# Optimization experiments

Measured on AMD Instinct MI355X. Metric: run time of the kernel, lower is better.

## Reference

```python
import jax, jax.numpy as jnp
import numpy as np

EMBED = 256
HEADS = 8
HEAD_DIM = EMBED // HEADS
LEVELS = 4
POINTS = 4
QUERY_DIM = 128
NQ = QUERY_DIM * QUERY_DIM
HIDDEN = 512
CHANNELS = [24, 40, 112, 1280]
SHAPES = [(64, 64), (32, 32), (16, 16), (8, 8)]
EPS = 1e-5


def group_norm(x, g, b, groups=32, eps=EPS):
    B, C, H, W = x.shape
    xr = x.reshape(B, groups, C // groups, H, W)
    mu = xr.mean(axis=(2, 3, 4), keepdims=True)
    var = xr.var(axis=(2, 3, 4), keepdims=True)
    xn = ((xr - mu) / jnp.sqrt(var + eps)).reshape(B, C, H, W)
    return xn * g[:, None, None] + b[:, None, None]


def layer_norm(x, g, b, eps=EPS):
    mu = x.mean(-1, keepdims=True)
    var = x.var(-1, keepdims=True)
    return (x - mu) / jnp.sqrt(var + eps) * g + b


def _sample_level(v, loc):
    # v: (B, H8, hd, H, W) value for one level; loc: (B, nq, H8, P, 2) in [0,1]
    B, Hh, hd, H, W = v.shape
    nq, P = loc.shape[1], loc.shape[3]
    # grid_sample semantics, align_corners=False, zero padding
    x = loc[..., 0] * W - 0.5
    y = loc[..., 1] * H - 0.5
    x0 = jnp.floor(x)
    y0 = jnp.floor(y)
    dx = x - x0
    dy = y - y0
    x0i = x0.astype(jnp.int32)
    y0i = y0.astype(jnp.int32)
    vflat = v.reshape(B, Hh, hd, H * W)

    def gather(xi, yi):
        valid = ((xi >= 0) & (xi < W) & (yi >= 0) & (yi < H)).astype(v.dtype)
        idx = jnp.clip(yi, 0, H - 1) * W + jnp.clip(xi, 0, W - 1)
        idxr = idx.transpose(0, 2, 1, 3).reshape(B, Hh, 1, nq * P)
        g = jnp.take_along_axis(vflat, idxr, axis=3).reshape(B, Hh, hd, nq, P)
        return g * valid.transpose(0, 2, 1, 3)[:, :, None]

    g00 = gather(x0i, y0i)
    g01 = gather(x0i + 1, y0i)
    g10 = gather(x0i, y0i + 1)
    g11 = gather(x0i + 1, y0i + 1)
    wx = dx.transpose(0, 2, 1, 3)[:, :, None]  # (B,H8,1,nq,P)
    wy = dy.transpose(0, 2, 1, 3)[:, :, None]
    return g00 * (1 - wx) * (1 - wy) + g01 * wx * (1 - wy) + g10 * (1 - wx) * wy + g11 * wx * wy


def reference(Q, grd0, grd1, grd2, grd3, batch_size,
              proj_w0, proj_b0, gn_g0, gn_b0,
              proj_w1, proj_b1, gn_g1, gn_b1,
              proj_w2, proj_b2, gn_g2, gn_b2,
              proj_w3, proj_b3, gn_g3, gn_b3,
              value_w, value_b, off_w, off_b, attw_w, attw_b,
              out_w, out_b, lin1_w, lin1_b, lin2_w, lin2_b, ln_g, ln_b):
    grd = [grd0, grd1, grd2, grd3]
    proj_w = [proj_w0, proj_w1, proj_w2, proj_w3]
    proj_b = [proj_b0, proj_b1, proj_b2, proj_b3]
    gn_g = [gn_g0, gn_g1, gn_g2, gn_g3]
    gn_b = [gn_b0, gn_b1, gn_b2, gn_b3]

    B = Q.shape[0]
    # project each level to embed dims (1x1 conv + GroupNorm) and flatten
    feats = []
    for l in range(LEVELS):
        f = jnp.einsum('bchw,co->bohw', grd[l], proj_w[l]) + proj_b[l][:, None, None]
        f = group_norm(f, gn_g[l], gn_b[l])
        feats.append(f.reshape(B, EMBED, -1).transpose(0, 2, 1))  # (B, H*W, E)
    value = jnp.concatenate(feats, axis=1)  # (B, NV, E)

    # reference points: meshgrid 'xy' over linspace(0,1,query_dim), shape (1,nq,1,2)
    lin = jnp.linspace(0.0, 1.0, QUERY_DIM)
    gx, gy = jnp.meshgrid(lin, lin, indexing='xy')
    ref = jnp.stack([gx, gy], axis=-1).reshape(1, NQ, 1, 2)

    # MSDeformAttn (mmcv): value proj, sampling offsets, attention weights
    v = (value @ value_w + value_b).reshape(B, -1, HEADS, HEAD_DIM)
    offs = (Q @ off_w + off_b).reshape(B, NQ, HEADS, LEVELS, POINTS, 2)
    aw = (Q @ attw_w + attw_b).reshape(B, NQ, HEADS, LEVELS * POINTS)
    aw = jax.nn.softmax(aw, axis=-1).reshape(B, NQ, HEADS, LEVELS, POINTS)

    # offset normalizer: (W, H) per level
    norm = jnp.array([[w, h] for (h, w) in SHAPES], dtype=Q.dtype)  # (L,2)
    # sampling_locations: (B,nq,H8,L,P,2); ref broadcasts over heads/levels/points
    loc = ref[:, :, None, :, None, :] + offs / norm[None, None, None, :, None, :]

    starts = np.concatenate([[0], np.cumsum([h * w for h, w in SHAPES])])
    out = jnp.zeros((B, HEADS, HEAD_DIM, NQ), dtype=Q.dtype)
    for l, (H, W) in enumerate(SHAPES):
        vl = v[:, starts[l]:starts[l + 1]].transpose(0, 2, 3, 1).reshape(B, HEADS, HEAD_DIM, H, W)
        sampled = _sample_level(vl, loc[:, :, :, l])  # (B,H8,hd,nq,P)
        out = out + jnp.einsum('bhdqp,bqhp->bhdq', sampled, aw[:, :, :, l])
    attn = out.transpose(0, 3, 1, 2).reshape(B, NQ, EMBED)
    attn = attn @ out_w + out_b
    attn = attn + Q  # mmcv internal residual (dropout is identity in eval)

    fused = attn + Q
    ffn = layer_norm(jax.nn.relu(fused @ lin1_w + lin1_b) @ lin2_w + lin2_b, ln_g, ln_b)
    return fused + ffn


def setup_inputs() -> dict:
    key = jax.random.key(0)
    ks = jax.random.split(key, 40)
    B = 4
    d = {
        'Q': jax.random.normal(ks[0], (B, NQ, EMBED), jnp.float32),
        'grd0': jax.random.normal(ks[1], (B, 24, 64, 64), jnp.float32),
        'grd1': jax.random.normal(ks[2], (B, 40, 32, 32), jnp.float32),
        'grd2': jax.random.normal(ks[3], (B, 112, 16, 16), jnp.float32),
        'grd3': jax.random.normal(ks[4], (B, 1280, 8, 8), jnp.float32),
        'batch_size': B,
    }
    i = 5
    for l, c in enumerate(CHANNELS):
        d[f'proj_w{l}'] = jax.random.normal(ks[i], (c, EMBED), jnp.float32) * (1.0 / np.sqrt(c)); i += 1
        d[f'proj_b{l}'] = jnp.zeros((EMBED,), jnp.float32)
        d[f'gn_g{l}'] = jnp.ones((EMBED,), jnp.float32)
        d[f'gn_b{l}'] = jnp.zeros((EMBED,), jnp.float32)

    def lin(k, fin, fout, scale=1.0):
        return jax.random.normal(k, (fin, fout), jnp.float32) * (scale / np.sqrt(fin))

    d['value_w'] = lin(ks[i], EMBED, EMBED); i += 1
    d['value_b'] = jnp.zeros((EMBED,), jnp.float32)
    d['off_w'] = lin(ks[i], EMBED, HEADS * LEVELS * POINTS * 2, 0.1); i += 1
    d['off_b'] = jnp.zeros((HEADS * LEVELS * POINTS * 2,), jnp.float32)
    d['attw_w'] = lin(ks[i], EMBED, HEADS * LEVELS * POINTS); i += 1
    d['attw_b'] = jnp.zeros((HEADS * LEVELS * POINTS,), jnp.float32)
    d['out_w'] = lin(ks[i], EMBED, EMBED); i += 1
    d['out_b'] = jnp.zeros((EMBED,), jnp.float32)
    d['lin1_w'] = lin(ks[i], EMBED, HIDDEN); i += 1
    d['lin1_b'] = jnp.zeros((HIDDEN,), jnp.float32)
    d['lin2_w'] = lin(ks[i], HIDDEN, EMBED); i += 1
    d['lin2_b'] = jnp.zeros((EMBED,), jnp.float32)
    d['ln_g'] = jnp.ones((EMBED,), jnp.float32)
    d['ln_b'] = jnp.zeros((EMBED,), jnp.float32)
    return d
```

## Files before the change

kernel.cpp:

```cpp
#include <hip/hip_runtime.h>
#include <hip/hip_bf16.h>


#define NQc 16384
#define NVc 5440

typedef __attribute__((ext_vector_type(8))) short short8;
typedef __attribute__((ext_vector_type(4))) short short4v;
typedef __attribute__((ext_vector_type(4))) float f32x4;

__device__ __forceinline__ float wred(float v) {
#pragma unroll
  for (int o = 32; o > 0; o >>= 1) v += __shfl_down(v, o);
  return v;
}

__global__ __launch_bounds__(256) void tcast_kernel(
    const float* __restrict__ w, __hip_bfloat16* __restrict__ wt, int K, int N) {
  int i = blockIdx.x * 256 + threadIdx.x;
  if (i < K * N) {
    int k = i / N, n = i - k * N;
    wt[(size_t)n * K + k] = __float2bfloat16(w[i]);
  }
}

__global__ __launch_bounds__(256) void proj_kernel(
    const float* __restrict__ g0, const float* __restrict__ g1,
    const float* __restrict__ g2, const float* __restrict__ g3,
    const float* __restrict__ w0, const float* __restrict__ w1,
    const float* __restrict__ w2, const float* __restrict__ w3,
    const float* __restrict__ pb0, const float* __restrict__ pb1,
    const float* __restrict__ pb2, const float* __restrict__ pb3,
    float* __restrict__ val) {
  const int bid = blockIdx.x;
  const int b = bid / NVc;
  const int nv = bid - b * NVc;
  const float* gsrc; const float* w; const float* pb; int C, HW, hw;
  if (nv < 4096)      { gsrc = g0; w = w0; pb = pb0; C = 24;   HW = 4096; hw = nv; }
  else if (nv < 5120) { gsrc = g1; w = w1; pb = pb1; C = 40;   HW = 1024; hw = nv - 4096; }
  else if (nv < 5376) { gsrc = g2; w = w2; pb = pb2; C = 112;  HW = 256;  hw = nv - 5120; }
  else                { gsrc = g3; w = w3; pb = pb3; C = 1280; HW = 64;   hw = nv - 5376; }
  const int e = threadIdx.x;
  const float* gp = gsrc + (size_t)b * C * HW + hw;
  float a0 = 0.f, a1 = 0.f, a2 = 0.f, a3 = 0.f;
  for (int c = 0; c < C; c += 4) {
    float x0 = gp[(size_t)(c + 0) * HW];
    float x1 = gp[(size_t)(c + 1) * HW];
    float x2 = gp[(size_t)(c + 2) * HW];
    float x3 = gp[(size_t)(c + 3) * HW];
    a0 += x0 * w[(c + 0) * 256 + e];
    a1 += x1 * w[(c + 1) * 256 + e];
    a2 += x2 * w[(c + 2) * 256 + e];
    a3 += x3 * w[(c + 3) * 256 + e];
  }
  val[(size_t)bid * 256 + e] = (a0 + a1) + (a2 + a3) + pb[e];
}

__global__ __launch_bounds__(256) void gn_kernel(
    const float* __restrict__ val, __hip_bfloat16* __restrict__ valb,
    const float* __restrict__ gg0, const float* __restrict__ gb0,
    const float* __restrict__ gg1, const float* __restrict__ gb1,
    const float* __restrict__ gg2, const float* __restrict__ gb2,
    const float* __restrict__ gg3, const float* __restrict__ gb3) {
  const int bid = blockIdx.x;
  const int grp = bid & 31;
  const int l = (bid >> 5) & 3;
  const int b = bid >> 7;
  int HW, start; const float *gg, *gbeta;
  if (l == 0)      { HW = 4096; start = 0;    gg = gg0; gbeta = gb0; }
  else if (l == 1) { HW = 1024; start = 4096; gg = gg1; gbeta = gb1; }
  else if (l == 2) { HW = 256;  start = 5120; gg = gg2; gbeta = gb2; }
  else             { HW = 64;   start = 5376; gg = gg3; gbeta = gb3; }
  const int n = HW * 8;
  const size_t base = ((size_t)(b * NVc + start)) * 256 + grp * 8;
  float s = 0.f, s2 = 0.f;
  for (int i = threadIdx.x; i < n; i += 256) {
    float x = val[base + (size_t)(i >> 3) * 256 + (i & 7)];
    s += x; s2 += x * x;
  }
  s = wred(s); s2 = wred(s2);
  __shared__ float red[8];
  const int wv = threadIdx.x >> 6;
  if ((threadIdx.x & 63) == 0) { red[wv] = s; red[4 + wv] = s2; }
  __syncthreads();
  const float S = red[0] + red[1] + red[2] + red[3];
  const float S2 = red[4] + red[5] + red[6] + red[7];
  const float inv_n = 1.f / (float)n;
  const float mu = S * inv_n;
  const float var = S2 * inv_n - mu * mu;
  const float rstd = rsqrtf(var + 1e-5f);
  for (int i = threadIdx.x; i < n; i += 256) {
    const int j = i & 7;
    const int e = grp * 8 + j;
    const size_t idx = base + (size_t)(i >> 3) * 256 + j;
    const float y = (val[idx] - mu) * rstd * gg[e] + gbeta[e];
    valb[idx] = __float2bfloat16(y);
  }
}

template <int MODE, bool XF32>
__global__ __launch_bounds__(256) void gemm_bt(
    const void* __restrict__ Xv, const __hip_bfloat16* __restrict__ Wt,
    const float* __restrict__ bias, float* __restrict__ Cf,
    __hip_bfloat16* __restrict__ Cb, const float* __restrict__ Qres,
    int M, int N, int K) {
  const int m0 = blockIdx.x * 128;
  const int n0 = blockIdx.y * 128;
  const int tid = threadIdx.x;
  const int wave = tid >> 6;
  const int lane = tid & 63;
  const int wm = wave >> 1;
  const int wn = wave & 1;
  const int l15 = lane & 15;
  const int l4 = lane >> 4;
  __shared__ __align__(16) __hip_bfloat16 As[128 * 64];
  __shared__ __align__(16) __hip_bfloat16 Bs[128 * 64];
  f32x4 acc[4][4];
#pragma unroll
  for (int m = 0; m < 4; ++m)
#pragma unroll
    for (int n = 0; n < 4; ++n) acc[m][n] = (f32x4){0.f, 0.f, 0.f, 0.f};

  for (int k0 = 0; k0 < K; k0 += 64) {
#pragma unroll
    for (int j = 0; j < 4; ++j) {
      const int e = (j * 256 + tid) * 8;
      const int r = e >> 6;
      const int k = e & 63;
      if constexpr (XF32) {
        const float* Xf = (const float*)Xv;
        const float4 a = *reinterpret_cast<const float4*>(&Xf[(size_t)(m0 + r) * K + k0 + k]);
        const float4 b = *reinterpret_cast<const float4*>(&Xf[(size_t)(m0 + r) * K + k0 + k + 4]);
        union { __hip_bfloat16 h[8]; short8 v; } u;
        u.h[0] = __float2bfloat16(a.x); u.h[1] = __float2bfloat16(a.y);
        u.h[2] = __float2bfloat16(a.z); u.h[3] = __float2bfloat16(a.w);
        u.h[4] = __float2bfloat16(b.x); u.h[5] = __float2bfloat16(b.y);
        u.h[6] = __float2bfloat16(b.z); u.h[7] = __float2bfloat16(b.w);
        *reinterpret_cast<short8*>(&As[e]) = u.v;
      } else {
        const __hip_bfloat16* Xb = (const __hip_bfloat16*)Xv;
        *reinterpret_cast<short8*>(&As[e]) =
            *reinterpret_cast<const short8*>(&Xb[(size_t)(m0 + r) * K + k0 + k]);
      }
      *reinterpret_cast<short8*>(&Bs[e]) =
          *reinterpret_cast<const short8*>(&Wt[(size_t)(n0 + r) * K + k0 + k]);
    }
    __syncthreads();
#pragma unroll
    for (int ks = 0; ks < 2; ++ks) {
      short8 a[4], bfr[4];
#pragma unroll
      for (int m = 0; m < 4; ++m)
        a[m] = *reinterpret_cast<const short8*>(
            &As[(wm * 64 + m * 16 + l15) * 64 + ks * 32 + l4 * 8]);
#pragma unroll
      for (int n = 0; n < 4; ++n)
        bfr[n] = *reinterpret_cast<const short8*>(
            &Bs[(wn * 64 + n * 16 + l15) * 64 + ks * 32 + l4 * 8]);
#pragma unroll
      for (int m = 0; m < 4; ++m)
#pragma unroll
        for (int n = 0; n < 4; ++n)
          acc[m][n] = __builtin_amdgcn_mfma_f32_16x16x32_bf16(a[m], bfr[n], acc[m][n], 0, 0, 0);
    }
    __syncthreads();
  }

#pragma unroll
  for (int m = 0; m < 4; ++m) {
    const int row0 = m0 + wm * 64 + m * 16 + l4 * 4;
#pragma unroll
    for (int n = 0; n < 4; ++n) {
      const int col = n0 + wn * 64 + n * 16 + l15;
      const float bv = bias[col];
#pragma unroll
      for (int r = 0; r < 4; ++r) {
        const size_t ci = (size_t)(row0 + r) * N + col;
        float f = acc[m][n][r] + bv;
        if (MODE == 0) {
          Cf[ci] = f;
        } else if (MODE == 1) {
          Cb[ci] = __float2bfloat16(fmaxf(f, 0.f));
        } else if (MODE == 2) {
          f += 2.f * Qres[ci];
          Cf[ci] = f;
          Cb[ci] = __float2bfloat16(f);
        } else {
          Cb[ci] = __float2bfloat16(f);
        }
      }
    }
  }
}

__global__ __launch_bounds__(256) void softmax_kernel(float* __restrict__ aw) {
  const size_t t = (size_t)blockIdx.x * 256 + threadIdx.x;
  float* p = aw + t * 16;
  float v[16];
  *reinterpret_cast<float4*>(&v[0])  = *reinterpret_cast<const float4*>(p + 0);
  *reinterpret_cast<float4*>(&v[4])  = *reinterpret_cast<const float4*>(p + 4);
  *reinterpret_cast<float4*>(&v[8])  = *reinterpret_cast<const float4*>(p + 8);
  *reinterpret_cast<float4*>(&v[12]) = *reinterpret_cast<const float4*>(p + 12);
  float mx = v[0];
#pragma unroll
  for (int j = 1; j < 16; ++j) mx = fmaxf(mx, v[j]);
  float sum = 0.f;
#pragma unroll
  for (int j = 0; j < 16; ++j) { v[j] = __expf(v[j] - mx); sum += v[j]; }
  const float inv = 1.f / sum;
#pragma unroll
  for (int j = 0; j < 16; ++j) v[j] *= inv;
  *reinterpret_cast<float4*>(p + 0)  = *reinterpret_cast<const float4*>(&v[0]);
  *reinterpret_cast<float4*>(p + 4)  = *reinterpret_cast<const float4*>(&v[4]);
  *reinterpret_cast<float4*>(p + 8)  = *reinterpret_cast<const float4*>(&v[8]);
  *reinterpret_cast<float4*>(p + 12) = *reinterpret_cast<const float4*>(&v[12]);
}

__global__ __launch_bounds__(256) void sampler_kernel(
    const float* __restrict__ V, const float* __restrict__ OFFS,
    const float* __restrict__ AW, __hip_bfloat16* __restrict__ ATT) {
  __shared__ int   sIdx[512 * 4];
  __shared__ float sW[512 * 4];
  const int blk = blockIdx.x;
  const int b = blk >> 12;
  const int q0 = (blk & 4095) << 2;
  const int bid0 = blk << 2;

  for (int j = threadIdx.x; j < 512; j += 256) {
    const int q   = j >> 7;
    const int h   = (j >> 4) & 7;
    const int tap = j & 15;
    const int l = tap >> 2, p = tap & 3;
    const int gq = bid0 + q;
    const int qq = q0 + q;
    const float rx = (float)(qq & 127) * (1.f / 127.f);
    const float ry = (float)(qq >> 7) * (1.f / 127.f);
    const float2 oxy = *reinterpret_cast<const float2*>(
        &OFFS[(size_t)gq * 256 + h * 32 + tap * 2]);
    const float aw = AW[(size_t)gq * 128 + h * 16 + tap];
    const int W = 64 >> l;
    const int start = (l & 2) ? ((l & 1) ? 5376 : 5120) : ((l & 1) ? 4096 : 0);
    const float fW = (float)W;
    const float x = rx * fW + oxy.x - 0.5f;
    const float y = ry * fW + oxy.y - 0.5f;
    const float x0f = floorf(x);
    const float y0f = floorf(y);
    const int x0 = (int)x0f;
    const int y0 = (int)y0f;
    const float dx = x - x0f;
    const float dy = y - y0f;
    const int x1 = x0 + 1, y1 = y0 + 1;
    const float mx0 = (x0 >= 0 && x0 < W) ? 1.f : 0.f;
    const float mx1 = (x1 >= 0 && x1 < W) ? 1.f : 0.f;
    const float my0 = (y0 >= 0 && y0 < W) ? 1.f : 0.f;
    const float my1 = (y1 >= 0 && y1 < W) ? 1.f : 0.f;
    const int x0c = min(max(x0, 0), W - 1);
    const int x1c = min(max(x1, 0), W - 1);
    const int y0c = min(max(y0, 0), W - 1);
    const int y1c = min(max(y1, 0), W - 1);
    int4 I;
    I.x = start + y0c * W + x0c;
    I.y = start + y0c * W + x1c;
    I.z = start + y1c * W + x0c;
    I.w = start + y1c * W + x1c;
    float4 Wv;
    Wv.x = aw * (1.f - dx) * (1.f - dy) * (mx0 * my0);
    Wv.y = aw * dx * (1.f - dy) * (mx1 * my0);
    Wv.z = aw * (1.f - dx) * dy * (mx0 * my1);
    Wv.w = aw * dx * dy * (mx1 * my1);
    *reinterpret_cast<int4*>(&sIdx[j * 4]) = I;
    *reinterpret_cast<float4*>(&sW[j * 4]) = Wv;
  }
  __syncthreads();

  const int q  = threadIdx.x >> 6;
  const int h  = (threadIdx.x >> 3) & 7;
  const int dq = threadIdx.x & 7;
  const float* vb = V + (size_t)b * (NVc * 256) + h * 32 + dq * 4;
  const int jbase = (q * 8 + h) * 16;
  f32x4 acc = (f32x4){0.f, 0.f, 0.f, 0.f};
#pragma unroll
  for (int tap = 0; tap < 16; ++tap) {
    const int4   I  = *reinterpret_cast<const int4*>(&sIdx[(jbase + tap) * 4]);
    const float4 Wv = *reinterpret_cast<const float4*>(&sW[(jbase + tap) * 4]);
    const f32x4 v00 = *reinterpret_cast<const f32x4*>(vb + ((size_t)I.x << 8));
    const f32x4 v01 = *reinterpret_cast<const f32x4*>(vb + ((size_t)I.y << 8));
    const f32x4 v10 = *reinterpret_cast<const f32x4*>(vb + ((size_t)I.z << 8));
    const f32x4 v11 = *reinterpret_cast<const f32x4*>(vb + ((size_t)I.w << 8));
    acc += v00 * Wv.x;
    acc += v01 * Wv.y;
    acc += v10 * Wv.z;
    acc += v11 * Wv.w;
  }
  union { __hip_bfloat16 hh[4]; short4v v; } u;
  u.hh[0] = __float2bfloat16(acc.x);
  u.hh[1] = __float2bfloat16(acc.y);
  u.hh[2] = __float2bfloat16(acc.z);
  u.hh[3] = __float2bfloat16(acc.w);
  *reinterpret_cast<short4v*>(
      &ATT[(size_t)(bid0 + q) * 256 + h * 32 + dq * 4]) = u.v;
}

__global__ __launch_bounds__(256) void ln_add_kernel(
    const __hip_bfloat16* __restrict__ T, const float* __restrict__ lng,
    const float* __restrict__ lnb, float* __restrict__ out) {
  const size_t row = blockIdx.x;
  const int e = threadIdx.x;
  const float t = __bfloat162float(T[row * 256 + e]);
  float s = wred(t);
  float s2 = wred(t * t);
  __shared__ float red[8];
  const int wv = e >> 6;
  if ((e & 63) == 0) { red[wv] = s; red[4 + wv] = s2; }
  __syncthreads();
  const float S = red[0] + red[1] + red[2] + red[3];
  const float S2 = red[4] + red[5] + red[6] + red[7];
  const float mu = S * (1.f / 256.f);
  const float var = S2 * (1.f / 256.f) - mu * mu;
  const float y = (t - mu) * rsqrtf(var + 1e-5f) * lng[e] + lnb[e];
  out[row * 256 + e] += y;
}

extern "C" void kernel_launch(void* const* d_in, const int* in_sizes, int n_in,
                              void* d_out, int out_size, void* d_ws, size_t ws_size,
                              hipStream_t stream) {
  const float* Q  = (const float*)d_in[0];
  const float* g0 = (const float*)d_in[1];
  const float* g1 = (const float*)d_in[2];
  const float* g2 = (const float*)d_in[3];
  const float* g3 = (const float*)d_in[4];
  const float* pw0 = (const float*)d_in[6];
  const float* pb0 = (const float*)d_in[7];
  const float* gg0 = (const float*)d_in[8];
  const float* gb0 = (const float*)d_in[9];
  const float* pw1 = (const float*)d_in[10];
  const float* pb1 = (const float*)d_in[11];
  const float* gg1 = (const float*)d_in[12];
  const float* gb1 = (const float*)d_in[13];
  const float* pw2 = (const float*)d_in[14];
  const float* pb2 = (const float*)d_in[15];
  const float* gg2 = (const float*)d_in[16];
  const float* gb2 = (const float*)d_in[17];
  const float* pw3 = (const float*)d_in[18];
  const float* pb3 = (const float*)d_in[19];
  const float* gg3 = (const float*)d_in[20];
  const float* gb3 = (const float*)d_in[21];
  const float* value_w = (const float*)d_in[22];
  const float* value_b = (const float*)d_in[23];
  const float* off_w   = (const float*)d_in[24];
  const float* off_b   = (const float*)d_in[25];
  const float* attw_w  = (const float*)d_in[26];
  const float* attw_b  = (const float*)d_in[27];
  const float* out_w   = (const float*)d_in[28];
  const float* out_b   = (const float*)d_in[29];
  const float* lin1_w  = (const float*)d_in[30];
  const float* lin1_b  = (const float*)d_in[31];
  const float* lin2_w  = (const float*)d_in[32];
  const float* lin2_b  = (const float*)d_in[33];
  const float* ln_g    = (const float*)d_in[34];
  const float* ln_b    = (const float*)d_in[35];

  char* ws = (char*)d_ws;
  __hip_bfloat16* WT_VALUE = (__hip_bfloat16*)(ws + 0);
  __hip_bfloat16* WT_OFF   = (__hip_bfloat16*)(ws + 131072);
  __hip_bfloat16* WT_ATTW  = (__hip_bfloat16*)(ws + 262144);
  __hip_bfloat16* WT_OUT   = (__hip_bfloat16*)(ws + 327680);
  __hip_bfloat16* WT_LIN1  = (__hip_bfloat16*)(ws + 458752);
  __hip_bfloat16* WT_LIN2  = (__hip_bfloat16*)(ws + 720896);
  float*          VAL      = (float*)(ws + 1048576);
  __hip_bfloat16* VALB     = (__hip_bfloat16*)(ws + 23330816);
  float*          V        = (float*)(ws + 34603008);
  float*          AW       = (float*)(ws + 56885248);
  __hip_bfloat16* ATT      = (__hip_bfloat16*)(ws + 1048576);
  __hip_bfloat16* FUSEDB   = (__hip_bfloat16*)(ws + 34603008);
  __hip_bfloat16* HIDH     = (__hip_bfloat16*)(ws + 1048576);
  __hip_bfloat16* T16H     = (__hip_bfloat16*)(ws + 68157440);
  float*          OFFS     = (float*)d_out;
  float*          FUSED    = (float*)d_out;

  tcast_kernel<<<256, 256, 0, stream>>>(value_w, WT_VALUE, 256, 256);
  tcast_kernel<<<256, 256, 0, stream>>>(off_w,   WT_OFF,   256, 256);
  tcast_kernel<<<128, 256, 0, stream>>>(attw_w,  WT_ATTW,  256, 128);
  tcast_kernel<<<256, 256, 0, stream>>>(out_w,   WT_OUT,   256, 256);
  tcast_kernel<<<512, 256, 0, stream>>>(lin1_w,  WT_LIN1,  256, 512);
  tcast_kernel<<<512, 256, 0, stream>>>(lin2_w,  WT_LIN2,  512, 256);

  proj_kernel<<<21760, 256, 0, stream>>>(g0, g1, g2, g3, pw0, pw1, pw2, pw3,
                                         pb0, pb1, pb2, pb3, VAL);
  gn_kernel<<<512, 256, 0, stream>>>(VAL, VALB, gg0, gb0, gg1, gb1, gg2, gb2, gg3, gb3);
  gemm_bt<0, false><<<dim3(170, 2), 256, 0, stream>>>(VALB, WT_VALUE, value_b, V,
                                                      nullptr, nullptr, 21760, 256, 256);

  gemm_bt<0, true><<<dim3(512, 2), 256, 0, stream>>>(Q, WT_OFF, off_b, OFFS,
                                                     nullptr, nullptr, 65536, 256, 256);
  gemm_bt<0, true><<<dim3(512, 1), 256, 0, stream>>>(Q, WT_ATTW, attw_b, AW,
                                                     nullptr, nullptr, 65536, 128, 256);
  softmax_kernel<<<2048, 256, 0, stream>>>(AW);

  sampler_kernel<<<16384, 256, 0, stream>>>(V, OFFS, AW, ATT);

  gemm_bt<2, false><<<dim3(512, 2), 256, 0, stream>>>(ATT, WT_OUT, out_b, FUSED,
                                                      FUSEDB, Q, 65536, 256, 256);

  for (int h = 0; h < 2; ++h) {
    const __hip_bfloat16* Xh = FUSEDB + (size_t)h * 32768 * 256;
    gemm_bt<1, false><<<dim3(256, 4), 256, 0, stream>>>(Xh, WT_LIN1, lin1_b, nullptr,
                                                        HIDH, nullptr, 32768, 512, 256);
    gemm_bt<3, false><<<dim3(256, 2), 256, 0, stream>>>(HIDH, WT_LIN2, lin2_b, nullptr,
                                                        T16H, nullptr, 32768, 256, 512);
    ln_add_kernel<<<32768, 256, 0, stream>>>(T16H, ln_g, ln_b,
                                             FUSED + (size_t)h * 32768 * 256);
  }
}
```

Before: 774.7 us.

## Replace scalar per-pixel projection with padded bf16 MFMA GEMMs per level

The fp32 scalar proj_kernel, one block per spatial position, is replaced by four bf16 GEMMs, one per feature level. Inputs are transposed and zero-padded to the GEMM K alignment, and the projection weights are cast and padded. The value buffer layout moves from batch-major to level-major, so the groupnorm and sampler indexing are rewritten to match, and the workspace offsets are reshuffled. This trades exact fp32 projection for bf16 precision and adds extra small transpose and pad launches, one of which runs a 1280-channel loop per thread on a single block.

```diff
diff --git a/kernel.cpp b/kernel.cpp
--- a/kernel.cpp
+++ b/kernel.cpp
@@ -24,36 +24,27 @@
   }
 }
 
-__global__ __launch_bounds__(256) void proj_kernel(
-    const float* __restrict__ g0, const float* __restrict__ g1,
-    const float* __restrict__ g2, const float* __restrict__ g3,
-    const float* __restrict__ w0, const float* __restrict__ w1,
-    const float* __restrict__ w2, const float* __restrict__ w3,
-    const float* __restrict__ pb0, const float* __restrict__ pb1,
-    const float* __restrict__ pb2, const float* __restrict__ pb3,
-    float* __restrict__ val) {
-  const int bid = blockIdx.x;
-  const int b = bid / NVc;
-  const int nv = bid - b * NVc;
-  const float* gsrc; const float* w; const float* pb; int C, HW, hw;
-  if (nv < 4096)      { gsrc = g0; w = w0; pb = pb0; C = 24;   HW = 4096; hw = nv; }
-  else if (nv < 5120) { gsrc = g1; w = w1; pb = pb1; C = 40;   HW = 1024; hw = nv - 4096; }
-  else if (nv < 5376) { gsrc = g2; w = w2; pb = pb2; C = 112;  HW = 256;  hw = nv - 5120; }
-  else                { gsrc = g3; w = w3; pb = pb3; C = 1280; HW = 64;   hw = nv - 5376; }
-  const int e = threadIdx.x;
-  const float* gp = gsrc + (size_t)b * C * HW + hw;
-  float a0 = 0.f, a1 = 0.f, a2 = 0.f, a3 = 0.f;
-  for (int c = 0; c < C; c += 4) {
-    float x0 = gp[(size_t)(c + 0) * HW];
-    float x1 = gp[(size_t)(c + 1) * HW];
-    float x2 = gp[(size_t)(c + 2) * HW];
-    float x3 = gp[(size_t)(c + 3) * HW];
-    a0 += x0 * w[(c + 0) * 256 + e];
-    a1 += x1 * w[(c + 1) * 256 + e];
-    a2 += x2 * w[(c + 2) * 256 + e];
-    a3 += x3 * w[(c + 3) * 256 + e];
-  }
-  val[(size_t)bid * 256 + e] = (a0 + a1) + (a2 + a3) + pb[e];
+__global__ __launch_bounds__(256) void tcast_pad_kernel(
+    const float* __restrict__ w, __hip_bfloat16* __restrict__ wt,
+    int K, int Kp, int N) {
+  int i = blockIdx.x * 256 + threadIdx.x;
+  if (i < N * Kp) {
+    int n = i / Kp, k = i - n * Kp;
+    wt[i] = (k < K) ? __float2bfloat16(w[k * N + n]) : __float2bfloat16(0.f);
+  }
+}
+
+__global__ __launch_bounds__(256) void tpad_kernel(
+    const float* __restrict__ grd, __hip_bfloat16* __restrict__ xp,
+    int C, int Kp, int HW) {
+  const int row = blockIdx.x * 256 + threadIdx.x;
+  const int b = row / HW;
+  const int hw = row - b * HW;
+  const float* g = grd + (size_t)b * C * HW + hw;
+  __hip_bfloat16* o = xp + (size_t)row * Kp;
+  int c = 0;
+  for (; c < C; ++c) o[c] = __float2bfloat16(g[(size_t)c * HW]);
+  for (; c < Kp; ++c) o[c] = __float2bfloat16(0.f);
 }
 
 __global__ __launch_bounds__(256) void gn_kernel(
@@ -66,13 +57,13 @@
   const int grp = bid & 31;
   const int l = (bid >> 5) & 3;
   const int b = bid >> 7;
-  int HW, start; const float *gg, *gbeta;
-  if (l == 0)      { HW = 4096; start = 0;    gg = gg0; gbeta = gb0; }
-  else if (l == 1) { HW = 1024; start = 4096; gg = gg1; gbeta = gb1; }
-  else if (l == 2) { HW = 256;  start = 5120; gg = gg2; gbeta = gb2; }
-  else             { HW = 64;   start = 5376; gg = gg3; gbeta = gb3; }
+  int HW, startB; const float *gg, *gbeta;
+  if (l == 0)      { HW = 4096; startB = 0;     gg = gg0; gbeta = gb0; }
+  else if (l == 1) { HW = 1024; startB = 16384; gg = gg1; gbeta = gb1; }
+  else if (l == 2) { HW = 256;  startB = 20480; gg = gg2; gbeta = gb2; }
+  else             { HW = 64;   startB = 21504; gg = gg3; gbeta = gb3; }
   const int n = HW * 8;
-  const size_t base = ((size_t)(b * NVc + start)) * 256 + grp * 8;
+  const size_t base = ((size_t)(startB + b * HW)) * 256 + grp * 8;
   float s = 0.f, s2 = 0.f;
   for (int i = threadIdx.x; i < n; i += 256) {
     float x = val[base + (size_t)(i >> 3) * 256 + (i & 7)];
@@ -230,7 +221,7 @@
     const int q   = j >> 7;
     const int h   = (j >> 4) & 7;
     const int tap = j & 15;
-    const int l = tap >> 2, p = tap & 3;
+    const int l = tap >> 2;
     const int gq = bid0 + q;
     const int qq = q0 + q;
     const float rx = (float)(qq & 127) * (1.f / 127.f);
@@ -239,7 +230,9 @@
         &OFFS[(size_t)gq * 256 + h * 32 + tap * 2]);
     const float aw = AW[(size_t)gq * 128 + h * 16 + tap];
     const int W = 64 >> l;
-    const int start = (l & 2) ? ((l & 1) ? 5376 : 5120) : ((l & 1) ? 4096 : 0);
+    const int HWl = W * W;
+    const int startB = (l == 0) ? 0 : (l == 1) ? 16384 : (l == 2) ? 20480 : 21504;
+    const int rowbase = startB + b * HWl;
     const float fW = (float)W;
     const float x = rx * fW + oxy.x - 0.5f;
     const float y = ry * fW + oxy.y - 0.5f;
@@ -259,10 +252,10 @@
     const int y0c = min(max(y0, 0), W - 1);
     const int y1c = min(max(y1, 0), W - 1);
     int4 I;
-    I.x = start + y0c * W + x0c;
-    I.y = start + y0c * W + x1c;
-    I.z = start + y1c * W + x0c;
-    I.w = start + y1c * W + x1c;
+    I.x = rowbase + y0c * W + x0c;
+    I.y = rowbase + y0c * W + x1c;
+    I.z = rowbase + y1c * W + x0c;
+    I.w = rowbase + y1c * W + x1c;
     float4 Wv;
     Wv.x = aw * (1.f - dx) * (1.f - dy) * (mx0 * my0);
     Wv.y = aw * dx * (1.f - dy) * (mx1 * my0);
@@ -276,7 +269,7 @@
   const int q  = threadIdx.x >> 6;
   const int h  = (threadIdx.x >> 3) & 7;
   const int dq = threadIdx.x & 7;
-  const float* vb = V + (size_t)b * (NVc * 256) + h * 32 + dq * 4;
+  const float* vb = V + h * 32 + dq * 4;
   const int jbase = (q * 8 + h) * 16;
   f32x4 acc = (f32x4){0.f, 0.f, 0.f, 0.f};
 #pragma unroll
@@ -367,14 +360,22 @@
   __hip_bfloat16* WT_OUT   = (__hip_bfloat16*)(ws + 327680);
   __hip_bfloat16* WT_LIN1  = (__hip_bfloat16*)(ws + 458752);
   __hip_bfloat16* WT_LIN2  = (__hip_bfloat16*)(ws + 720896);
-  float*          VAL      = (float*)(ws + 1048576);
-  __hip_bfloat16* VALB     = (__hip_bfloat16*)(ws + 23330816);
-  float*          V        = (float*)(ws + 34603008);
-  float*          AW       = (float*)(ws + 56885248);
-  __hip_bfloat16* ATT      = (__hip_bfloat16*)(ws + 1048576);
-  __hip_bfloat16* FUSEDB   = (__hip_bfloat16*)(ws + 34603008);
-  __hip_bfloat16* HIDH     = (__hip_bfloat16*)(ws + 1048576);
-  __hip_bfloat16* T16H     = (__hip_bfloat16*)(ws + 68157440);
+  __hip_bfloat16* WTP0     = (__hip_bfloat16*)(ws + 983040);
+  __hip_bfloat16* WTP1     = (__hip_bfloat16*)(ws + 1015808);
+  __hip_bfloat16* WTP2     = (__hip_bfloat16*)(ws + 1048576);
+  __hip_bfloat16* WTP3     = (__hip_bfloat16*)(ws + 1114112);
+  __hip_bfloat16* XP0      = (__hip_bfloat16*)(ws + 1769472);
+  __hip_bfloat16* XP1      = (__hip_bfloat16*)(ws + 3866624);
+  __hip_bfloat16* XP2      = (__hip_bfloat16*)(ws + 4390912);
+  __hip_bfloat16* XP3      = (__hip_bfloat16*)(ws + 4653056);
+  float*          VAL      = (float*)(ws + 34406400);
+  __hip_bfloat16* VALB     = (__hip_bfloat16*)(ws + 23265280);
+  float*          V        = (float*)(ws + 983040);
+  float*          AW       = (float*)(ws + 23265280);
+  __hip_bfloat16* ATT      = (__hip_bfloat16*)(ws + 56819712);
+  __hip_bfloat16* FUSEDB   = (__hip_bfloat16*)(ws + 983040);
+  __hip_bfloat16* HIDH     = (__hip_bfloat16*)(ws + 34537472);
+  __hip_bfloat16* T16H     = (__hip_bfloat16*)(ws + 68091904);
   float*          OFFS     = (float*)d_out;
   float*          FUSED    = (float*)d_out;
 
@@ -384,9 +385,24 @@
   tcast_kernel<<<256, 256, 0, stream>>>(out_w,   WT_OUT,   256, 256);
   tcast_kernel<<<512, 256, 0, stream>>>(lin1_w,  WT_LIN1,  256, 512);
   tcast_kernel<<<512, 256, 0, stream>>>(lin2_w,  WT_LIN2,  512, 256);
-
-  proj_kernel<<<21760, 256, 0, stream>>>(g0, g1, g2, g3, pw0, pw1, pw2, pw3,
-                                         pb0, pb1, pb2, pb3, VAL);
+  tcast_pad_kernel<<<64,   256, 0, stream>>>(pw0, WTP0, 24,   64,   256);
+  tcast_pad_kernel<<<64,   256, 0, stream>>>(pw1, WTP1, 40,   64,   256);
+  tcast_pad_kernel<<<128,  256, 0, stream>>>(pw2, WTP2, 112,  128,  256);
+  tcast_pad_kernel<<<1280, 256, 0, stream>>>(pw3, WTP3, 1280, 1280, 256);
+
+  tpad_kernel<<<64, 256, 0, stream>>>(g0, XP0, 24,   64,   4096);
+  tpad_kernel<<<16, 256, 0, stream>>>(g1, XP1, 40,   64,   1024);
+  tpad_kernel<<<4,  256, 0, stream>>>(g2, XP2, 112,  128,  256);
+  tpad_kernel<<<1,  256, 0, stream>>>(g3, XP3, 1280, 1280, 64);
+
+  gemm_bt<0, false><<<dim3(128, 2), 256, 0, stream>>>(XP0, WTP0, pb0, VAL,
+                                                      nullptr, nullptr, 16384, 256, 64);
+  gemm_bt<0, false><<<dim3(32, 2), 256, 0, stream>>>(XP1, WTP1, pb1, VAL + (size_t)16384 * 256,
+                                                     nullptr, nullptr, 4096, 256, 64);
+  gemm_bt<0, false><<<dim3(8, 2), 256, 0, stream>>>(XP2, WTP2, pb2, VAL + (size_t)20480 * 256,
+                                                    nullptr, nullptr, 1024, 256, 128);
+  gemm_bt<0, false><<<dim3(2, 2), 256, 0, stream>>>(XP3, WTP3, pb3, VAL + (size_t)21504 * 256,
+                                                    nullptr, nullptr, 256, 256, 1280);
   gn_kernel<<<512, 256, 0, stream>>>(VAL, VALB, gg0, gb0, gg1, gb1, gg2, gb2, gg3, gb3);
   gemm_bt<0, false><<<dim3(170, 2), 256, 0, stream>>>(VALB, WT_VALUE, value_b, V,
                                                       nullptr, nullptr, 21760, 256, 256);
```

After: 1.397 ms. +80.4%, slower.
